# Performance work log

Measured on AMD Instinct MI355X. Metric: run time of the kernel, lower is better.

Reference implementation:

```python
import jax, jax.numpy as jnp
import numpy as np

# Module hyperparameters (from init_kwargs)
H, W = 256, 256
NUM_ANGLE, NUM_RHO = 360, 360
MASK_WIDTH = 3.0
N, C = 16, 1


def setup_inputs() -> dict:
    key = jax.random.key(0)
    hough_map = jax.random.uniform(key, (N, C, NUM_ANGLE, NUM_RHO), dtype=jnp.float32)
    return {"hough_map": hough_map}


def _peak_mask(hough_map):
    # max_pool2d(k=3, s=1, p=1) local-max detection + 0.5*global-max threshold
    pooled = jax.lax.reduce_window(
        hough_map, -jnp.inf, jax.lax.max,
        window_dimensions=(1, 1, 3, 3), window_strides=(1, 1, 1, 1), padding="SAME")
    gmax = jnp.max(hough_map, axis=(-2, -1), keepdims=True)
    return (hough_map == pooled) & (hough_map > 0.5 * gmax)


def reference(hough_map):
    n, c, A, R = hough_map.shape
    peak = _peak_mask(hough_map).astype(jnp.float32)  # [N,C,A,R], 0/1

    # xy grid centered at image center (matches torch meshgrid indexing='ij')
    yv = jnp.arange(H, dtype=jnp.float32) - (H - 1) / 2
    xv = jnp.arange(W, dtype=jnp.float32) - (W - 1) / 2
    yy, xx = jnp.meshgrid(yv, xv, indexing="ij")
    xflat, yflat = xx.ravel(), yy.ravel()  # [H*W]

    delta_rho = 2.0 * float(np.sqrt((W / 2) ** 2 + (H / 2) ** 2)) / (NUM_RHO - 1)
    rho_vals = (jnp.arange(R, dtype=jnp.float32) - R / 2) * delta_rho  # [R]
    thetas = jnp.arange(A, dtype=jnp.float32) * (np.pi / NUM_ANGLE)    # [A]
    cos_t, sin_t = jnp.cos(thetas), jnp.sin(thetas)

    # Per (n,c): out = any over peaks (a,r) of |cos_a*x + sin_a*y - rho_r| < w.
    # Since peak/line masks are 0/1, max-over-peaks == (boolean matmul > 0).
    # Scan over angles to avoid materializing the [A,R,H*W] line tensor.
    peak_per_a = peak.reshape(n * c, A, R).transpose(1, 0, 2)  # [A, NC, R]

    def body(carry, inp):
        ct, st, pk = inp                       # pk: [NC, R]
        rho_cal = ct * xflat + st * yflat      # [HW]
        line = (jnp.abs(rho_cal[None, :] - rho_vals[:, None]) < MASK_WIDTH)
        hit = pk @ line.astype(jnp.float32)    # [NC, HW]
        return jnp.maximum(carry, jnp.where(hit > 0, 1.0, 0.0)), None

    init = jnp.zeros((n * c, H * W), jnp.float32)
    out, _ = jax.lax.scan(body, init, (cos_t, sin_t, peak_per_a))
    return out.reshape(n, c, H, W)
```

## Files before the change

kernel.cpp:

```cpp
#include <hip/hip_runtime.h>
#include <math.h>

#define NN 16
#define AA 360
#define RR 360
#define HH 256
#define WW 256
#define WORDS 7
#define BAND 8
#define NBAND (AA / BAND)
#define NBLK (NN * NBAND)
#define PTHR 384
#define CAP 16
#define OTHR 512

__device__ __forceinline__ bool fhit(float rc, int r, float drho) {
    const float rho = __fmul_rn((float)(r - 180), drho);
    return fabsf(__fsub_rn(rc, rho)) < 3.0f;
}

__global__ void __launch_bounds__(PTHR)
k_peaks(const float* __restrict__ h, float* __restrict__ part,
        float* __restrict__ tab, unsigned long long* __restrict__ bits,
        uint2* __restrict__ lowlist, float dtheta) {
    __shared__ float rows[BAND + 2][RR];
    __shared__ float s_red[6];
    __shared__ int s_cnt;
    const int blk  = blockIdx.x;
    const int n    = blk / NBAND;
    const int band = blk % NBAND;
    const int a0   = band * BAND;
    const int t    = threadIdx.x;

    if (t == 0) s_cnt = 0;

    if (a0 > 0 && a0 + BAND < AA) {
        const float4* src = (const float4*)(h + ((size_t)n * AA + a0 - 1) * RR);
        float4* dst = (float4*)&rows[0][0];
        for (int i = t; i < (BAND + 2) * RR / 4; i += PTHR) dst[i] = src[i];
    } else {
        for (int i = t; i < (BAND + 2) * RR; i += PTHR) {
            const int aa = a0 - 1 + i / RR;
            (&rows[0][0])[i] = (aa >= 0 && aa < AA)
                ? h[((size_t)n * AA + aa) * RR + (i - (i / RR) * RR)] : -INFINITY;
        }
    }
    if (blk == 0) {
        for (int a = t; a < AA; a += PTHR) {
            float th = __fmul_rn((float)a, dtheta);
            tab[a]      = (float)cos((double)th);
            tab[AA + a] = (float)sin((double)th);
        }
    }
    __syncthreads();

    {
        const float* cen = &rows[1][0];
        float m = 0.0f;
        for (int i = t; i < BAND * RR; i += PTHR) m = fmaxf(m, cen[i]);
        #pragma unroll
        for (int s = 32; s > 0; s >>= 1) m = fmaxf(m, __shfl_down(m, s, 64));
        if ((t & 63) == 0) s_red[t >> 6] = m;
        __syncthreads();
        if (t == 0) {
            m = s_red[0];
            #pragma unroll
            for (int i = 1; i < 6; ++i) m = fmaxf(m, s_red[i]);
            part[blk] = m;
        }
    }

    const int r = t;
    float hm[BAND + 2];
    if (r < RR) {
        #pragma unroll
        for (int j = 0; j < BAND + 2; ++j) {
            const float a_ = (r > 0)      ? rows[j][r - 1] : -INFINITY;
            const float c_ = (r < RR - 1) ? rows[j][r + 1] : -INFINITY;
            hm[j] = fmaxf(fmaxf(a_, rows[j][r]), c_);
        }
    }
    #pragma unroll
    for (int k = 0; k < BAND; ++k) {
        bool hi = false;
        if (r < RR) {
            const float v = rows[k + 1][r];
            const float pooled = fmaxf(fmaxf(hm[k], hm[k + 1]), hm[k + 2]);
            if (v >= pooled) {
                if (v >= 0.5f) hi = true;
                else {
                    const int slot = atomicAdd(&s_cnt, 1);
                    if (slot < CAP)
                        lowlist[blk * CAP + slot] =
                            make_uint2(((unsigned)(a0 + k) << 16) | (unsigned)r,
                                       __float_as_uint(v));
                }
            }
        }
        const unsigned long long m = __ballot(hi);
        if ((t & 63) == 0)
            bits[((size_t)n * AA + a0 + k) * WORDS + (t >> 6)] = m;
    }
    if (t < BAND)
        bits[((size_t)n * AA + a0 + t) * WORDS + 6] = 0ull;
    __syncthreads();
    for (int i = s_cnt + t; i < CAP; i += PTHR)
        lowlist[blk * CAP + i] = make_uint2(0u, 0u);
}

__global__ void __launch_bounds__(OTHR)
k_out(const unsigned long long* __restrict__ bits, const float* __restrict__ part,
      const float* __restrict__ tab, const uint2* __restrict__ lowlist,
      float* __restrict__ out, float inv_dr, float drho) {
    __shared__ __align__(16) unsigned long long Lb[AA * WORDS];
    __shared__ float Lct[AA], Lst[AA];
    __shared__ float s_gth;
    const int n     = blockIdx.x >> 6;
    const int chunk = blockIdx.x & 63;
    const int t     = threadIdx.x;

    if (t < 64) {
        float m = (t < NBAND) ? part[n * NBAND + t] : 0.0f;
        #pragma unroll
        for (int s = 32; s > 0; s >>= 1) m = fmaxf(m, __shfl_down(m, s, 64));
        if (t == 0) s_gth = 0.5f * m;
    }
    {
        const uint4* src = (const uint4*)(bits + (size_t)n * AA * WORDS);
        uint4* dst = (uint4*)Lb;
        for (int i = t; i < AA * WORDS / 2; i += OTHR) dst[i] = src[i];
        for (int i = t; i < AA; i += OTHR) {
            Lct[i] = tab[i];
            Lst[i] = tab[AA + i];
        }
    }
    __syncthreads();
    const float gth = s_gth;

    for (int i = t; i < NBAND * CAP; i += OTHR) {
        const uint2 e = lowlist[(size_t)n * NBAND * CAP + i];
        if (__uint_as_float(e.y) > gth) {
            const int a = e.x >> 16, r = e.x & 0xffff;
            atomicOr((unsigned int*)Lb + a * (WORDS * 2) + (r >> 5), 1u << (r & 31));
        }
    }
    __syncthreads();

    const int pbase = chunk * 1024 + t;
    #pragma unroll
    for (int q = 0; q < 2; ++q) {
        const int p = pbase + q * OTHR;
        const int y = p >> 8;
        const int x = p & 255;
        const float xf = (float)x - 127.5f;
        const float yf = (float)y - 127.5f;
        float res = 0.0f;
        for (int a = 0; a < AA; ++a) {
            const float rc = __fadd_rn(__fmul_rn(Lct[a], xf), __fmul_rn(Lst[a], yf));
            const int lo_est = (int)ceilf (__fmul_rn(__fsub_rn(rc, 3.0f), inv_dr)) + 180;
            const int hi_est = (int)floorf(__fmul_rn(__fadd_rn(rc, 3.0f), inv_dr)) + 180;
            int lo = fhit(rc, lo_est - 1, drho) ? lo_est - 1
                   : (fhit(rc, lo_est, drho) ? lo_est : lo_est + 1);
            int hi = fhit(rc, hi_est + 1, drho) ? hi_est + 1
                   : (fhit(rc, hi_est, drho) ? hi_est : hi_est - 1);
            lo = lo < 0 ? 0 : lo;
            hi = hi > RR - 1 ? RR - 1 : hi;
            if (lo <= hi) {
                const int len = hi - lo + 1;
                const unsigned long long pmask = (1ull << len) - 1ull;
                const int sh = lo & 63;
                const int w  = lo >> 6;
                const unsigned long long m0 = pmask << sh;
                const unsigned long long m1 = sh ? (pmask >> (64 - sh)) : 0ull;
                const unsigned long long v0 = Lb[a * WORDS + w];
                const unsigned long long v1 = Lb[a * WORDS + w + 1];
                if ((v0 & m0) | (v1 & m1)) { res = 1.0f; break; }
            }
        }
        out[(size_t)n * (HH * WW) + p] = res;
    }
}

extern "C" void kernel_launch(void* const* d_in, const int* in_sizes, int n_in,
                              void* d_out, int out_size, void* d_ws, size_t ws_size,
                              hipStream_t stream) {
    const float* h = (const float*)d_in[0];
    float* out = (float*)d_out;

    char* ws = (char*)d_ws;
    unsigned long long* bits = (unsigned long long*)ws;
    float* part = (float*)(ws + (size_t)NN * AA * WORDS * 8);
    float* tab  = part + NBLK;
    uint2* lowlist = (uint2*)(tab + 2 * AA);

    const double dr_d = 2.0 * sqrt((WW / 2.0) * (WW / 2.0) + (HH / 2.0) * (HH / 2.0)) / (RR - 1);
    const float drho   = (float)dr_d;
    const float inv_dr = (float)(1.0 / dr_d);
    const float dtheta = (float)(3.14159265358979323846 / 360.0);

    k_peaks<<<NBLK, PTHR, 0, stream>>>(h, part, tab, bits, lowlist, dtheta);
    k_out<<<NN * 64, OTHR, 0, stream>>>(bits, part, tab, lowlist, out, inv_dr, drho);
}
```

Baseline: 72.53 us.

## Fuse peak detection and line rendering into one kernel with per-image flag barrier

Merges the peak-finding and output kernels into a single launch. Each block publishes a release flag when its band is done, then spins until all bands of the same image are flagged before building the shared bitmask and rendering its own slice of pixels. The cos/sin table is now written per image by one block, and the shared buffers are overlaid in a union to limit LDS use. This removes the second launch and the gap between kernels. In exchange it needs every block to be co-resident and relies on flags that are never reset, so later calls can see stale MAGIC values and race with the previous call's data.

```diff
diff --git a/kernel.cpp b/kernel.cpp
--- a/kernel.cpp
+++ b/kernel.cpp
@@ -10,22 +10,30 @@
 #define BAND 8
 #define NBAND (AA / BAND)
 #define NBLK (NN * NBAND)
-#define PTHR 384
+#define NTHR 384
 #define CAP 16
-#define OTHR 512
+#define CHUNK 1457
+#define MAGIC 0x17C3A55Au
 
 __device__ __forceinline__ bool fhit(float rc, int r, float drho) {
     const float rho = __fmul_rn((float)(r - 180), drho);
     return fabsf(__fsub_rn(rc, rho)) < 3.0f;
 }
 
-__global__ void __launch_bounds__(PTHR)
-k_peaks(const float* __restrict__ h, float* __restrict__ part,
-        float* __restrict__ tab, unsigned long long* __restrict__ bits,
-        uint2* __restrict__ lowlist, float dtheta) {
-    __shared__ float rows[BAND + 2][RR];
+__global__ void __launch_bounds__(NTHR, 8)
+k_all(const float* __restrict__ h, float* __restrict__ part,
+      unsigned long long* __restrict__ bits, uint2* __restrict__ lowlist,
+      float* __restrict__ tab, unsigned int* __restrict__ flags,
+      float* __restrict__ out, float dtheta, float drho, float inv_dr) {
+    __shared__ __align__(16) union {
+        float rows[BAND + 2][RR];
+        struct { unsigned long long Lb[AA * WORDS]; } c;
+    } S;
+    __shared__ float Lct[AA], Lst[AA];
     __shared__ float s_red[6];
+    __shared__ float s_gth;
     __shared__ int s_cnt;
+
     const int blk  = blockIdx.x;
     const int n    = blk / NBAND;
     const int band = blk % NBAND;
@@ -36,28 +44,29 @@
 
     if (a0 > 0 && a0 + BAND < AA) {
         const float4* src = (const float4*)(h + ((size_t)n * AA + a0 - 1) * RR);
-        float4* dst = (float4*)&rows[0][0];
-        for (int i = t; i < (BAND + 2) * RR / 4; i += PTHR) dst[i] = src[i];
+        float4* dst = (float4*)&S.rows[0][0];
+        for (int i = t; i < (BAND + 2) * RR / 4; i += NTHR) dst[i] = src[i];
     } else {
-        for (int i = t; i < (BAND + 2) * RR; i += PTHR) {
+        for (int i = t; i < (BAND + 2) * RR; i += NTHR) {
             const int aa = a0 - 1 + i / RR;
-            (&rows[0][0])[i] = (aa >= 0 && aa < AA)
+            (&S.rows[0][0])[i] = (aa >= 0 && aa < AA)
                 ? h[((size_t)n * AA + aa) * RR + (i - (i / RR) * RR)] : -INFINITY;
         }
     }
-    if (blk == 0) {
-        for (int a = t; a < AA; a += PTHR) {
+    if (band == 1) {
+        float* tn = tab + (size_t)n * 2 * AA;
+        for (int a = t; a < AA; a += NTHR) {
             float th = __fmul_rn((float)a, dtheta);
-            tab[a]      = (float)cos((double)th);
-            tab[AA + a] = (float)sin((double)th);
+            tn[a]      = (float)cos((double)th);
+            tn[AA + a] = (float)sin((double)th);
         }
     }
     __syncthreads();
 
     {
-        const float* cen = &rows[1][0];
+        const float* cen = &S.rows[1][0];
         float m = 0.0f;
-        for (int i = t; i < BAND * RR; i += PTHR) m = fmaxf(m, cen[i]);
+        for (int i = t; i < BAND * RR; i += NTHR) m = fmaxf(m, cen[i]);
         #pragma unroll
         for (int s = 32; s > 0; s >>= 1) m = fmaxf(m, __shfl_down(m, s, 64));
         if ((t & 63) == 0) s_red[t >> 6] = m;
@@ -75,16 +84,16 @@
     if (r < RR) {
         #pragma unroll
         for (int j = 0; j < BAND + 2; ++j) {
-            const float a_ = (r > 0)      ? rows[j][r - 1] : -INFINITY;
-            const float c_ = (r < RR - 1) ? rows[j][r + 1] : -INFINITY;
-            hm[j] = fmaxf(fmaxf(a_, rows[j][r]), c_);
+            const float a_ = (r > 0)      ? S.rows[j][r - 1] : -INFINITY;
+            const float c_ = (r < RR - 1) ? S.rows[j][r + 1] : -INFINITY;
+            hm[j] = fmaxf(fmaxf(a_, S.rows[j][r]), c_);
         }
     }
     #pragma unroll
     for (int k = 0; k < BAND; ++k) {
         bool hi = false;
         if (r < RR) {
-            const float v = rows[k + 1][r];
+            const float v = S.rows[k + 1][r];
             const float pooled = fmaxf(fmaxf(hm[k], hm[k + 1]), hm[k + 2]);
             if (v >= pooled) {
                 if (v >= 0.5f) hi = true;
@@ -104,20 +113,28 @@
     if (t < BAND)
         bits[((size_t)n * AA + a0 + t) * WORDS + 6] = 0ull;
     __syncthreads();
-    for (int i = s_cnt + t; i < CAP; i += PTHR)
+    for (int i = s_cnt + t; i < CAP; i += NTHR)
         lowlist[blk * CAP + i] = make_uint2(0u, 0u);
-}
-
-__global__ void __launch_bounds__(OTHR)
-k_out(const unsigned long long* __restrict__ bits, const float* __restrict__ part,
-      const float* __restrict__ tab, const uint2* __restrict__ lowlist,
-      float* __restrict__ out, float inv_dr, float drho) {
-    __shared__ __align__(16) unsigned long long Lb[AA * WORDS];
-    __shared__ float Lct[AA], Lst[AA];
-    __shared__ float s_gth;
-    const int n     = blockIdx.x >> 6;
-    const int chunk = blockIdx.x & 63;
-    const int t     = threadIdx.x;
+    __syncthreads();
+
+    if (t == 0) {
+        __threadfence();
+        __hip_atomic_store(&flags[blk], MAGIC, __ATOMIC_RELEASE,
+                           __HIP_MEMORY_SCOPE_AGENT);
+    }
+
+    if (t < 64) {
+        const unsigned int* f = flags + n * NBAND;
+        bool done = (t >= NBAND);
+        for (;;) {
+            if (!done)
+                done = (__hip_atomic_load(&f[t], __ATOMIC_ACQUIRE,
+                                          __HIP_MEMORY_SCOPE_AGENT) == MAGIC);
+            if (__all(done)) break;
+            __builtin_amdgcn_s_sleep(1);
+        }
+    }
+    __syncthreads();
 
     if (t < 64) {
         float m = (t < NBAND) ? part[n * NBAND + t] : 0.0f;
@@ -127,29 +144,30 @@
     }
     {
         const uint4* src = (const uint4*)(bits + (size_t)n * AA * WORDS);
-        uint4* dst = (uint4*)Lb;
-        for (int i = t; i < AA * WORDS / 2; i += OTHR) dst[i] = src[i];
-        for (int i = t; i < AA; i += OTHR) {
-            Lct[i] = tab[i];
-            Lst[i] = tab[AA + i];
+        uint4* dst = (uint4*)S.c.Lb;
+        for (int i = t; i < AA * WORDS / 2; i += NTHR) dst[i] = src[i];
+        const float* tn = tab + (size_t)n * 2 * AA;
+        for (int i = t; i < AA; i += NTHR) {
+            Lct[i] = tn[i];
+            Lst[i] = tn[AA + i];
         }
     }
     __syncthreads();
     const float gth = s_gth;
 
-    for (int i = t; i < NBAND * CAP; i += OTHR) {
+    for (int i = t; i < NBAND * CAP; i += NTHR) {
         const uint2 e = lowlist[(size_t)n * NBAND * CAP + i];
         if (__uint_as_float(e.y) > gth) {
-            const int a = e.x >> 16, r = e.x & 0xffff;
-            atomicOr((unsigned int*)Lb + a * (WORDS * 2) + (r >> 5), 1u << (r & 31));
-        }
-    }
-    __syncthreads();
-
-    const int pbase = chunk * 1024 + t;
-    #pragma unroll
-    for (int q = 0; q < 2; ++q) {
-        const int p = pbase + q * OTHR;
+            const int a = e.x >> 16, rr = e.x & 0xffff;
+            atomicOr((unsigned int*)S.c.Lb + a * (WORDS * 2) + (rr >> 5),
+                     1u << (rr & 31));
+        }
+    }
+    __syncthreads();
+
+    const int pbeg = band * CHUNK;
+    const int pend = (pbeg + CHUNK < HH * WW) ? (pbeg + CHUNK) : (HH * WW);
+    for (int p = pbeg + t; p < pend; p += NTHR) {
         const int y = p >> 8;
         const int x = p & 255;
         const float xf = (float)x - 127.5f;
@@ -172,8 +190,8 @@
                 const int w  = lo >> 6;
                 const unsigned long long m0 = pmask << sh;
                 const unsigned long long m1 = sh ? (pmask >> (64 - sh)) : 0ull;
-                const unsigned long long v0 = Lb[a * WORDS + w];
-                const unsigned long long v1 = Lb[a * WORDS + w + 1];
+                const unsigned long long v0 = S.c.Lb[a * WORDS + w];
+                const unsigned long long v1 = S.c.Lb[a * WORDS + w + 1];
                 if ((v0 & m0) | (v1 & m1)) { res = 1.0f; break; }
             }
         }
@@ -190,14 +208,15 @@
     char* ws = (char*)d_ws;
     unsigned long long* bits = (unsigned long long*)ws;
     float* part = (float*)(ws + (size_t)NN * AA * WORDS * 8);
-    float* tab  = part + NBLK;
-    uint2* lowlist = (uint2*)(tab + 2 * AA);
+    uint2* lowlist = (uint2*)(part + NBLK);
+    float* tab = (float*)(lowlist + NBLK * CAP);
+    unsigned int* flags = (unsigned int*)(tab + NN * 2 * AA);
 
     const double dr_d = 2.0 * sqrt((WW / 2.0) * (WW / 2.0) + (HH / 2.0) * (HH / 2.0)) / (RR - 1);
     const float drho   = (float)dr_d;
     const float inv_dr = (float)(1.0 / dr_d);
     const float dtheta = (float)(3.14159265358979323846 / 360.0);
 
-    k_peaks<<<NBLK, PTHR, 0, stream>>>(h, part, tab, bits, lowlist, dtheta);
-    k_out<<<NN * 64, OTHR, 0, stream>>>(bits, part, tab, lowlist, out, inv_dr, drho);
+    k_all<<<NBLK, NTHR, 0, stream>>>(h, part, bits, lowlist, tab, flags, out,
+                                     dtheta, drho, inv_dr);
 }
```

New measurement: 108.6 us. 1.5x slower.
